# Performance work log

Measured on AMD Instinct MI355X. Metric: run time of the kernel, lower is better.

## Reference

```python
import jax, jax.numpy as jnp
import numpy as np

DECAY = 0.99
EPSILON = 1e-05
CODEBOOK_SIZE = 1024


def setup_inputs() -> dict:
    key = jax.random.key(0)
    k1, k2, k3 = jax.random.split(key, 3)
    B, T, D, K = 8, 4096, 128, CODEBOOK_SIZE
    return {
        "x": jax.random.normal(k1, (B, T, D), dtype=jnp.float32),
        "embed": jax.random.normal(k2, (K, D), dtype=jnp.float32),
        "cluster_size": jnp.ones((K,), dtype=jnp.float32),
        "embed_avg": jax.random.normal(k3, (K, D), dtype=jnp.float32),
    }


def reference(x, embed, cluster_size, embed_avg):
    shape = x.shape
    K, D = embed.shape
    flat = x.reshape(-1, D)  # (N, D)

    dist = 2.0 * (flat @ embed.T) - jnp.sum(flat * flat, axis=1, keepdims=True) \
           - jnp.sum(embed * embed, axis=1)[None, :]  # (N, K)
    embed_ind_flat = jnp.argmax(dist, axis=-1)  # (N,) int
    embed_ind = embed_ind_flat.reshape(shape[:-1])
    quantize = embed[embed_ind]  # dequantize via gather, (B, T, D)

    # training EMA updates (one-hot scatter expressed as segment sums)
    counts = jax.ops.segment_sum(jnp.ones_like(embed_ind_flat, dtype=x.dtype),
                                 embed_ind_flat, num_segments=K)  # == onehot.sum(0)
    embed_sum = jax.ops.segment_sum(flat, embed_ind_flat, num_segments=K)  # == (x.T @ onehot).T

    new_cluster_size = cluster_size * DECAY + (1.0 - DECAY) * counts
    new_embed_avg = embed_avg * DECAY + (1.0 - DECAY) * embed_sum

    total = new_cluster_size.sum()
    smoothed = (new_cluster_size + EPSILON) / (total + K * EPSILON) * total
    new_embed = new_embed_avg / smoothed[:, None]

    return quantize, embed_ind, new_cluster_size, new_embed_avg, new_embed
```

## Files before the change

kernel.cpp:

```cpp
#include <hip/hip_runtime.h>

#define NROWS 32768
#define DDIM  128
#define KCODES 1024
#define DECAY 0.99f
#define OMD   0.01f
#define EPS   1e-5f

typedef __attribute__((ext_vector_type(8))) short short8;
typedef __attribute__((ext_vector_type(4))) float f32x4;

#define WS_COUNTS 0
#define WS_OFFS   1024
#define WS_CURSOR 2048
#define WS_INV    3072
#define WS_EN2H   4096
#define WS_BUCKET 5120

__device__ __forceinline__ unsigned int f2bf(float f) {
  union { float f; unsigned int u; } cv; cv.f = f;
  unsigned int u = cv.u;
  return (u + 0x7fffu + ((u >> 16) & 1u)) >> 16;
}

__device__ __forceinline__ void gload16(const void* g, void* l) {
  __builtin_amdgcn_global_load_lds(
      (const __attribute__((address_space(1))) unsigned int*)g,
      (__attribute__((address_space(3))) unsigned int*)l, 16, 0, 0);
}

__global__ __launch_bounds__(256) void pack_e(const float* __restrict__ embed,
                                              ushort* __restrict__ epack,
                                              float* __restrict__ en2h,
                                              int* __restrict__ cnt0) {
  const int tid = threadIdx.x;
  const int nt = blockIdx.x;
  if (nt == 0) {
    #pragma unroll
    for (int i = 0; i < 4; ++i) cnt0[tid + i * 256] = 0;
  }
  const int m = tid >> 4, s = tid & 15;
  const int kb = s >> 2, q = s & 3;
  const int row = nt * 16 + m;
  const float* ep = embed + (size_t)row * DDIM + kb * 32 + q * 8;
  float4 v0 = *(const float4*)(ep);
  float4 v1 = *(const float4*)(ep + 4);
  float v[8] = {v0.x, v0.y, v0.z, v0.w, v1.x, v1.y, v1.z, v1.w};
  unsigned int h[8], l[8];
  float ss = 0.f;
  #pragma unroll
  for (int j = 0; j < 8; ++j) {
    ss += v[j] * v[j];
    h[j] = f2bf(v[j]);
    float fh = __uint_as_float(h[j] << 16);
    l[j] = f2bf(v[j] - fh);
  }
  uint4 ph, pl;
  ph.x = h[0] | (h[1] << 16); ph.y = h[2] | (h[3] << 16);
  ph.z = h[4] | (h[5] << 16); ph.w = h[6] | (h[7] << 16);
  pl.x = l[0] | (l[1] << 16); pl.y = l[2] | (l[3] << 16);
  pl.z = l[4] | (l[5] << 16); pl.w = l[6] | (l[7] << 16);
  *(uint4*)(epack + (((size_t)nt * 8 + kb) * 64 + q * 16 + m) * 8)     = ph;
  *(uint4*)(epack + (((size_t)nt * 8 + kb + 4) * 64 + q * 16 + m) * 8) = pl;
  ss += __shfl_xor(ss, 1, 64);
  ss += __shfl_xor(ss, 2, 64);
  ss += __shfl_xor(ss, 4, 64);
  ss += __shfl_xor(ss, 8, 64);
  if (s == 0) en2h[row] = 0.5f * ss;
}

__global__ __launch_bounds__(512, 2) void vq_mfma(
    const float* __restrict__ x, const short8* __restrict__ ep8,
    const float* __restrict__ en2h, const float* __restrict__ embed,
    float* __restrict__ out_ind, float* __restrict__ out_q,
    int* __restrict__ cnt_i) {
  __shared__ short8 bfrag[2][512];
  __shared__ float nlds[KCODES];
  __shared__ int scodes[128];
  const int tid = threadIdx.x;
  const int w = tid >> 6, lane = tid & 63;
  const int c = lane & 15, q = lane >> 4;
  const int row0 = blockIdx.x * 128;

  gload16(ep8 + w * 64 + lane, &bfrag[0][w * 64]);
  nlds[tid]       = en2h[tid];
  nlds[tid + 512] = en2h[tid + 512];

  short8 a[8];
  {
    const float* xp = x + (size_t)(row0 + w * 16 + c) * DDIM + q * 8;
    #pragma unroll
    for (int kb = 0; kb < 4; ++kb) {
      float4 v0 = *(const float4*)(xp + kb * 32);
      float4 v1 = *(const float4*)(xp + kb * 32 + 4);
      float v[8] = {v0.x, v0.y, v0.z, v0.w, v1.x, v1.y, v1.z, v1.w};
      short8 hh, ll;
      #pragma unroll
      for (int j = 0; j < 8; ++j) {
        unsigned int hv = f2bf(v[j]);
        hh[j] = (short)hv;
        float fh = __uint_as_float(hv << 16);
        ll[j] = (short)f2bf(v[j] - fh);
      }
      a[kb] = hh;
      a[kb + 4] = ll;
    }
  }

  float bestv[4]; int besti[4];
  #pragma unroll
  for (int i = 0; i < 4; ++i) { bestv[i] = -3.4e38f; besti[i] = 0; }

  asm volatile("s_waitcnt vmcnt(0)" ::: "memory");
  __syncthreads();

  for (int nt = 0; nt < 64; ++nt) {
    const int cur = nt & 1;
    if (nt < 63)
      gload16(ep8 + (size_t)(nt + 1) * 512 + w * 64 + lane,
              &bfrag[cur ^ 1][w * 64]);
    __builtin_amdgcn_sched_barrier(0);

    short8 st[8];
    #pragma unroll
    for (int j = 0; j < 8; ++j) st[j] = bfrag[cur][j * 64 + lane];
    const float nh = nlds[nt * 16 + c];

    f32x4 accA = {-nh, -nh, -nh, -nh};
    f32x4 accB = {0.f, 0.f, 0.f, 0.f};
    f32x4 accC = {0.f, 0.f, 0.f, 0.f};
    __builtin_amdgcn_s_setprio(1);
    #pragma unroll
    for (int kb = 0; kb < 4; ++kb) {
      accA = __builtin_amdgcn_mfma_f32_16x16x32_bf16(a[kb],     st[kb],     accA, 0, 0, 0);
      accB = __builtin_amdgcn_mfma_f32_16x16x32_bf16(a[kb + 4], st[kb],     accB, 0, 0, 0);
      accC = __builtin_amdgcn_mfma_f32_16x16x32_bf16(a[kb],     st[kb + 4], accC, 0, 0, 0);
    }
    __builtin_amdgcn_s_setprio(0);

    const int code = nt * 16 + c;
    #pragma unroll
    for (int r = 0; r < 4; ++r) {
      float s = accA[r] + accB[r] + accC[r];
      if (s > bestv[r]) { bestv[r] = s; besti[r] = code; }
    }

    asm volatile("s_waitcnt vmcnt(0)" ::: "memory");
    __syncthreads();
  }

  #pragma unroll
  for (int off = 1; off < 16; off <<= 1) {
    #pragma unroll
    for (int i = 0; i < 4; ++i) {
      float ov = __shfl_xor(bestv[i], off, 64);
      int   oi = __shfl_xor(besti[i], off, 64);
      if (ov > bestv[i] || (ov == bestv[i] && oi < besti[i])) {
        bestv[i] = ov; besti[i] = oi;
      }
    }
  }
  if (c == 0) {
    #pragma unroll
    for (int r = 0; r < 4; ++r) {
      const int row = w * 16 + q * 4 + r;
      out_ind[row0 + row] = (float)besti[r];
      scodes[row] = besti[r];
      atomicAdd(&cnt_i[besti[r]], 1);
    }
  }
  __syncthreads();
  #pragma unroll
  for (int it = 0; it < 8; ++it) {
    int idx = tid + it * 512;
    int row = idx >> 5, c4 = idx & 31;
    int code = scodes[row];
    *(float4*)(out_q + (size_t)(row0 + row) * DDIM + c4 * 4) =
        *(const float4*)(embed + (size_t)code * DDIM + c4 * 4);
  }
}

__global__ __launch_bounds__(1024) void scan_fin(
    int* offs, const float* __restrict__ cs,
    float* __restrict__ counts_g, int* __restrict__ cursor,
    float* __restrict__ inv, float* __restrict__ out_ncs) {
  __shared__ float wtot[16], ctot[16];
  const int tid = threadIdx.x;
  const int lane = tid & 63, w = tid >> 6;
  const int cnt = offs[tid];
  const float cnum = (float)cnt;
  const float cv = cs[tid];
  float s = cnum;
  #pragma unroll
  for (int off = 1; off < 64; off <<= 1) {
    float v = __shfl_up(s, off, 64);
    if (lane >= off) s += v;
  }
  float r2 = cv;
  #pragma unroll
  for (int off = 32; off > 0; off >>= 1) r2 += __shfl_down(r2, off, 64);
  if (lane == 63) wtot[w] = s;
  if (lane == 0)  ctot[w] = r2;
  __syncthreads();
  if (tid < 16) {
    float v = wtot[tid];
    #pragma unroll
    for (int off = 1; off < 16; off <<= 1) {
      float p = __shfl_up(v, off, 64);
      if (tid >= off) v += p;
    }
    wtot[tid] = v;
    float t2 = ctot[tid];
    #pragma unroll
    for (int off = 8; off > 0; off >>= 1) t2 += __shfl_down(t2, off, 64);
    if (tid == 0) ctot[0] = t2;
  }
  __syncthreads();
  const float prefix = (w > 0) ? wtot[w - 1] : 0.f;
  const int excl = (int)(s + prefix) - cnt;
  offs[tid] = excl;
  cursor[tid] = excl;
  counts_g[tid] = cnum;
  const float ncs = cv * DECAY + OMD * cnum;
  out_ncs[tid] = ncs;
  const float total = ctot[0] * DECAY + OMD * (float)NROWS;
  inv[tid] = (total + (float)KCODES * EPS) / ((ncs + EPS) * total);
}

__global__ void scatter_rows(const float* __restrict__ out_ind,
                             int* __restrict__ cursor, int* __restrict__ bucket) {
  int row = blockIdx.x * 256 + threadIdx.x;
  int code = (int)out_ind[row];
  int pos = atomicAdd(cursor + code, 1);
  bucket[pos] = row;
}

__global__ __launch_bounds__(256) void esum_fin(
    const int* __restrict__ bucket, const int* __restrict__ offs,
    const float* __restrict__ counts, const float* __restrict__ x,
    const float* __restrict__ ea, const float* __restrict__ inv,
    float* __restrict__ out_nea, float* __restrict__ out_ne) {
  __shared__ float4 part[512];
  const int code = blockIdx.x;
  const int t = threadIdx.x;
  const int c8 = t & 15;
  const int h = t >> 4;
  const int start = offs[code];
  const int cnt = (int)counts[code];
  float4 a0 = {0.f, 0.f, 0.f, 0.f}, a1 = {0.f, 0.f, 0.f, 0.f};
  int i = h;
  for (; i + 16 < cnt; i += 32) {
    int rowA = bucket[start + i];
    int rowB = bucket[start + i + 16];
    const float* pa = x + (size_t)rowA * DDIM + c8 * 8;
    const float* pb = x + (size_t)rowB * DDIM + c8 * 8;
    float4 xa0 = *(const float4*)(pa), xa1 = *(const float4*)(pa + 4);
    float4 xb0 = *(const float4*)(pb), xb1 = *(const float4*)(pb + 4);
    a0.x += xa0.x + xb0.x; a0.y += xa0.y + xb0.y; a0.z += xa0.z + xb0.z; a0.w += xa0.w + xb0.w;
    a1.x += xa1.x + xb1.x; a1.y += xa1.y + xb1.y; a1.z += xa1.z + xb1.z; a1.w += xa1.w + xb1.w;
  }
  for (; i < cnt; i += 16) {
    int row = bucket[start + i];
    const float* pa = x + (size_t)row * DDIM + c8 * 8;
    float4 xa0 = *(const float4*)(pa), xa1 = *(const float4*)(pa + 4);
    a0.x += xa0.x; a0.y += xa0.y; a0.z += xa0.z; a0.w += xa0.w;
    a1.x += xa1.x; a1.y += xa1.y; a1.z += xa1.z; a1.w += xa1.w;
  }
  part[h * 32 + c8 * 2]     = a0;
  part[h * 32 + c8 * 2 + 1] = a1;
  __syncthreads();
  if (t < 32) {
    float4 s = part[t];
    #pragma unroll
    for (int hh = 1; hh < 16; ++hh) {
      float4 p = part[hh * 32 + t];
      s.x += p.x; s.y += p.y; s.z += p.z; s.w += p.w;
    }
    float iv = inv[code];
    int base = code * DDIM + t * 4;
    float4 a = *(const float4*)(ea + base);
    float4 nea;
    nea.x = a.x * DECAY + OMD * s.x; nea.y = a.y * DECAY + OMD * s.y;
    nea.z = a.z * DECAY + OMD * s.z; nea.w = a.w * DECAY + OMD * s.w;
    *(float4*)(out_nea + base) = nea;
    float4 ne;
    ne.x = nea.x * iv; ne.y = nea.y * iv; ne.z = nea.z * iv; ne.w = nea.w * iv;
    *(float4*)(out_ne + base) = ne;
  }
}

extern "C" void kernel_launch(void* const* d_in, const int* in_sizes, int n_in,
                              void* d_out, int out_size, void* d_ws, size_t ws_size,
                              hipStream_t stream) {
  const float* x     = (const float*)d_in[0];
  const float* embed = (const float*)d_in[1];
  const float* cs    = (const float*)d_in[2];
  const float* ea    = (const float*)d_in[3];

  float* out     = (float*)d_out;
  float* out_q   = out;
  float* out_ind = out_q + 4194304;
  float* out_ncs = out_ind + 32768;
  float* out_nea = out_ncs + 1024;
  float* out_ne  = out_nea + 131072;

  float* ws     = (float*)d_ws;
  float* counts = ws + WS_COUNTS;
  int*   offs   = (int*)(ws + WS_OFFS);
  int*   cursor = (int*)(ws + WS_CURSOR);
  float* inv    = ws + WS_INV;
  float* en2h   = ws + WS_EN2H;
  int*   bucket = (int*)(ws + WS_BUCKET);

  ushort* epack = (ushort*)out_nea;

  pack_e<<<64, 256, 0, stream>>>(embed, epack, en2h, offs);
  vq_mfma<<<NROWS / 128, 512, 0, stream>>>(x, (const short8*)epack, en2h, embed,
                                           out_ind, out_q, offs);
  scan_fin<<<1, 1024, 0, stream>>>(offs, cs, counts, cursor, inv, out_ncs);
  scatter_rows<<<NROWS / 256, 256, 0, stream>>>(out_ind, cursor, bucket);
  esum_fin<<<KCODES, 256, 0, stream>>>(bucket, offs, counts, x, ea, inv,
                                       out_nea, out_ne);
}
```

Measured before the change: 187.2 us.

## Halve vq block threads, give each wave two row tiles, deepen codebook prefetch

The distance kernel now runs 256 threads per block, and each wave handles 32 rows (two 16-row A tiles). Each B fragment loaded from LDS therefore feeds twice as many MFMAs. The codebook staging buffer grows from double to quad buffering, with a 3-tile-ahead prefetch throttled by vmcnt and raw s_barrier instead of a full wait-plus-syncthreads every tile. The aim is to cut LDS reads and barrier stalls per MFMA, at the cost of more registers per thread and fewer waves per block.

```diff
diff --git a/kernel.cpp b/kernel.cpp
--- a/kernel.cpp
+++ b/kernel.cpp
@@ -69,12 +69,12 @@
   if (s == 0) en2h[row] = 0.5f * ss;
 }
 
-__global__ __launch_bounds__(512, 2) void vq_mfma(
+__global__ __launch_bounds__(256, 2) void vq_mfma(
     const float* __restrict__ x, const short8* __restrict__ ep8,
     const float* __restrict__ en2h, const float* __restrict__ embed,
     float* __restrict__ out_ind, float* __restrict__ out_q,
     int* __restrict__ cnt_i) {
-  __shared__ short8 bfrag[2][512];
+  __shared__ short8 bfrag[4][512];
   __shared__ float nlds[KCODES];
   __shared__ int scodes[128];
   const int tid = threadIdx.x;
@@ -82,13 +82,12 @@
   const int c = lane & 15, q = lane >> 4;
   const int row0 = blockIdx.x * 128;
 
-  gload16(ep8 + w * 64 + lane, &bfrag[0][w * 64]);
-  nlds[tid]       = en2h[tid];
-  nlds[tid + 512] = en2h[tid + 512];
-
-  short8 a[8];
-  {
-    const float* xp = x + (size_t)(row0 + w * 16 + c) * DDIM + q * 8;
+  float4 nv = *(const float4*)(en2h + tid * 4);
+
+  short8 a[2][8];
+  #pragma unroll
+  for (int t = 0; t < 2; ++t) {
+    const float* xp = x + (size_t)(row0 + w * 32 + t * 16 + c) * DDIM + q * 8;
     #pragma unroll
     for (int kb = 0; kb < 4; ++kb) {
       float4 v0 = *(const float4*)(xp + kb * 32);
@@ -102,57 +101,83 @@
         float fh = __uint_as_float(hv << 16);
         ll[j] = (short)f2bf(v[j] - fh);
       }
-      a[kb] = hh;
-      a[kb + 4] = ll;
-    }
-  }
-
-  float bestv[4]; int besti[4];
-  #pragma unroll
-  for (int i = 0; i < 4; ++i) { bestv[i] = -3.4e38f; besti[i] = 0; }
-
-  asm volatile("s_waitcnt vmcnt(0)" ::: "memory");
-  __syncthreads();
-
-  for (int nt = 0; nt < 64; ++nt) {
-    const int cur = nt & 1;
-    if (nt < 63)
-      gload16(ep8 + (size_t)(nt + 1) * 512 + w * 64 + lane,
-              &bfrag[cur ^ 1][w * 64]);
-    __builtin_amdgcn_sched_barrier(0);
-
+      a[t][kb] = hh;
+      a[t][kb + 4] = ll;
+    }
+  }
+  *(float4*)(&nlds[tid * 4]) = nv;
+
+  #pragma unroll
+  for (int p = 0; p < 3; ++p) {
+    gload16(ep8 + (size_t)p * 512 + w * 64 + lane, &bfrag[p][w * 64]);
+    gload16(ep8 + (size_t)p * 512 + 256 + w * 64 + lane, &bfrag[p][256 + w * 64]);
+  }
+  asm volatile("s_waitcnt lgkmcnt(0)" ::: "memory");
+
+  float bestv[8]; int besti[8];
+  #pragma unroll
+  for (int i = 0; i < 8; ++i) { bestv[i] = -3.4e38f; besti[i] = 0; }
+
+  auto tile_compute = [&](int nt) {
+    const int cur = nt & 3;
     short8 st[8];
     #pragma unroll
     for (int j = 0; j < 8; ++j) st[j] = bfrag[cur][j * 64 + lane];
     const float nh = nlds[nt * 16 + c];
-
-    f32x4 accA = {-nh, -nh, -nh, -nh};
-    f32x4 accB = {0.f, 0.f, 0.f, 0.f};
-    f32x4 accC = {0.f, 0.f, 0.f, 0.f};
+    f32x4 accA0 = {-nh, -nh, -nh, -nh};
+    f32x4 accA1 = accA0;
+    f32x4 accB0 = {0.f, 0.f, 0.f, 0.f};
+    f32x4 accB1 = {0.f, 0.f, 0.f, 0.f};
+    f32x4 accC0 = {0.f, 0.f, 0.f, 0.f};
+    f32x4 accC1 = {0.f, 0.f, 0.f, 0.f};
     __builtin_amdgcn_s_setprio(1);
     #pragma unroll
     for (int kb = 0; kb < 4; ++kb) {
-      accA = __builtin_amdgcn_mfma_f32_16x16x32_bf16(a[kb],     st[kb],     accA, 0, 0, 0);
-      accB = __builtin_amdgcn_mfma_f32_16x16x32_bf16(a[kb + 4], st[kb],     accB, 0, 0, 0);
-      accC = __builtin_amdgcn_mfma_f32_16x16x32_bf16(a[kb],     st[kb + 4], accC, 0, 0, 0);
+      accA0 = __builtin_amdgcn_mfma_f32_16x16x32_bf16(a[0][kb],     st[kb],     accA0, 0, 0, 0);
+      accA1 = __builtin_amdgcn_mfma_f32_16x16x32_bf16(a[1][kb],     st[kb],     accA1, 0, 0, 0);
+      accB0 = __builtin_amdgcn_mfma_f32_16x16x32_bf16(a[0][kb + 4], st[kb],     accB0, 0, 0, 0);
+      accB1 = __builtin_amdgcn_mfma_f32_16x16x32_bf16(a[1][kb + 4], st[kb],     accB1, 0, 0, 0);
+      accC0 = __builtin_amdgcn_mfma_f32_16x16x32_bf16(a[0][kb],     st[kb + 4], accC0, 0, 0, 0);
+      accC1 = __builtin_amdgcn_mfma_f32_16x16x32_bf16(a[1][kb],     st[kb + 4], accC1, 0, 0, 0);
     }
     __builtin_amdgcn_s_setprio(0);
-
     const int code = nt * 16 + c;
     #pragma unroll
     for (int r = 0; r < 4; ++r) {
-      float s = accA[r] + accB[r] + accC[r];
-      if (s > bestv[r]) { bestv[r] = s; besti[r] = code; }
-    }
-
-    asm volatile("s_waitcnt vmcnt(0)" ::: "memory");
-    __syncthreads();
-  }
+      float s0 = accA0[r] + accB0[r] + accC0[r];
+      if (s0 > bestv[r])     { bestv[r] = s0;     besti[r] = code; }
+      float s1 = accA1[r] + accB1[r] + accC1[r];
+      if (s1 > bestv[4 + r]) { bestv[4 + r] = s1; besti[4 + r] = code; }
+    }
+  };
+
+  for (int nt = 0; nt < 61; ++nt) {
+    asm volatile("s_waitcnt vmcnt(4)" ::: "memory");
+    __builtin_amdgcn_s_barrier();
+    __builtin_amdgcn_sched_barrier(0);
+    const int bs = (nt + 3) & 3;
+    gload16(ep8 + (size_t)(nt + 3) * 512 + w * 64 + lane, &bfrag[bs][w * 64]);
+    gload16(ep8 + (size_t)(nt + 3) * 512 + 256 + w * 64 + lane, &bfrag[bs][256 + w * 64]);
+    __builtin_amdgcn_sched_barrier(0);
+    tile_compute(nt);
+  }
+  asm volatile("s_waitcnt vmcnt(4)" ::: "memory");
+  __builtin_amdgcn_s_barrier();
+  __builtin_amdgcn_sched_barrier(0);
+  tile_compute(61);
+  asm volatile("s_waitcnt vmcnt(2)" ::: "memory");
+  __builtin_amdgcn_s_barrier();
+  __builtin_amdgcn_sched_barrier(0);
+  tile_compute(62);
+  asm volatile("s_waitcnt vmcnt(0)" ::: "memory");
+  __builtin_amdgcn_s_barrier();
+  __builtin_amdgcn_sched_barrier(0);
+  tile_compute(63);
 
   #pragma unroll
   for (int off = 1; off < 16; off <<= 1) {
     #pragma unroll
-    for (int i = 0; i < 4; ++i) {
+    for (int i = 0; i < 8; ++i) {
       float ov = __shfl_xor(bestv[i], off, 64);
       int   oi = __shfl_xor(besti[i], off, 64);
       if (ov > bestv[i] || (ov == bestv[i] && oi < besti[i])) {
@@ -162,17 +187,20 @@
   }
   if (c == 0) {
     #pragma unroll
-    for (int r = 0; r < 4; ++r) {
-      const int row = w * 16 + q * 4 + r;
-      out_ind[row0 + row] = (float)besti[r];
-      scodes[row] = besti[r];
-      atomicAdd(&cnt_i[besti[r]], 1);
-    }
+    for (int t = 0; t < 2; ++t)
+      #pragma unroll
+      for (int r = 0; r < 4; ++r) {
+        const int row = w * 32 + t * 16 + q * 4 + r;
+        const int bi = besti[t * 4 + r];
+        out_ind[row0 + row] = (float)bi;
+        scodes[row] = bi;
+        atomicAdd(&cnt_i[bi], 1);
+      }
   }
   __syncthreads();
   #pragma unroll
-  for (int it = 0; it < 8; ++it) {
-    int idx = tid + it * 512;
+  for (int it = 0; it < 16; ++it) {
+    int idx = tid + it * 256;
     int row = idx >> 5, c4 = idx & 31;
     int code = scodes[row];
     *(float4*)(out_q + (size_t)(row0 + row) * DDIM + c4 * 4) =
@@ -315,7 +343,7 @@
   ushort* epack = (ushort*)out_nea;
 
   pack_e<<<64, 256, 0, stream>>>(embed, epack, en2h, offs);
-  vq_mfma<<<NROWS / 128, 512, 0, stream>>>(x, (const short8*)epack, en2h, embed,
+  vq_mfma<<<NROWS / 128, 256, 0, stream>>>(x, (const short8*)epack, en2h, embed,
                                            out_ind, out_q, offs);
   scan_fin<<<1, 1024, 0, stream>>>(offs, cs, counts, cursor, inv, out_ncs);
   scatter_rows<<<NROWS / 256, 256, 0, stream>>>(out_ind, cursor, bucket);
```

Result: no change. 190.6 us (+1.8%).

## Split codebook across wave halves with 4-stage prefetch and merge argmax keys

Applied to the files above, without the earlier changes.

The VQ kernel now processes 64 rows per block instead of 128. The two halves of its 8 waves each scan half of the codebook (32 tiles), so twice as many blocks run and each wave does half the serial tile loop. Codebook fragments are prefetched through a 4-deep LDS ring with counted vmcnt waits and raw s_barrier, replacing the double buffer that waited on every load each iteration. The per-half argmax results are merged through packed 64-bit order-preserving keys that keep lowest-index tie-breaking. Launch bounds ask for 4 blocks per CU, which caps registers and raises LDS use per block.

```diff
diff --git a/kernel.cpp b/kernel.cpp
--- a/kernel.cpp
+++ b/kernel.cpp
@@ -69,26 +69,25 @@
   if (s == 0) en2h[row] = 0.5f * ss;
 }
 
-__global__ __launch_bounds__(512, 2) void vq_mfma(
+__global__ __launch_bounds__(512, 4) void vq_mfma(
     const float* __restrict__ x, const short8* __restrict__ ep8,
     const float* __restrict__ en2h, const float* __restrict__ embed,
     float* __restrict__ out_ind, float* __restrict__ out_q,
     int* __restrict__ cnt_i) {
-  __shared__ short8 bfrag[2][512];
+  __shared__ short8 bfrag[2][4][512];
   __shared__ float nlds[KCODES];
-  __shared__ int scodes[128];
+  __shared__ unsigned long long keys[2][64];
+  __shared__ int scodes[64];
   const int tid = threadIdx.x;
   const int w = tid >> 6, lane = tid & 63;
+  const int h = w >> 2, r = w & 3;
   const int c = lane & 15, q = lane >> 4;
-  const int row0 = blockIdx.x * 128;
-
-  gload16(ep8 + w * 64 + lane, &bfrag[0][w * 64]);
-  nlds[tid]       = en2h[tid];
-  nlds[tid + 512] = en2h[tid + 512];
+  const int row0 = blockIdx.x * 64;
+  const int nt0 = h * 32;
 
   short8 a[8];
   {
-    const float* xp = x + (size_t)(row0 + w * 16 + c) * DDIM + q * 8;
+    const float* xp = x + (size_t)(row0 + r * 16 + c) * DDIM + q * 8;
     #pragma unroll
     for (int kb = 0; kb < 4; ++kb) {
       float4 v0 = *(const float4*)(xp + kb * 32);
@@ -106,26 +105,28 @@
       a[kb + 4] = ll;
     }
   }
+  nlds[tid]       = en2h[tid];
+  nlds[tid + 512] = en2h[tid + 512];
+
+  __builtin_amdgcn_sched_barrier(0);
+  #pragma unroll
+  for (int p = 0; p < 3; ++p) {
+    gload16(ep8 + (size_t)(nt0 + p) * 512 + r * 128 + lane,
+            &bfrag[h][p][r * 128]);
+    gload16(ep8 + (size_t)(nt0 + p) * 512 + r * 128 + 64 + lane,
+            &bfrag[h][p][r * 128 + 64]);
+  }
+  asm volatile("s_waitcnt lgkmcnt(0)" ::: "memory");
 
   float bestv[4]; int besti[4];
   #pragma unroll
   for (int i = 0; i < 4; ++i) { bestv[i] = -3.4e38f; besti[i] = 0; }
 
-  asm volatile("s_waitcnt vmcnt(0)" ::: "memory");
-  __syncthreads();
-
-  for (int nt = 0; nt < 64; ++nt) {
-    const int cur = nt & 1;
-    if (nt < 63)
-      gload16(ep8 + (size_t)(nt + 1) * 512 + w * 64 + lane,
-              &bfrag[cur ^ 1][w * 64]);
-    __builtin_amdgcn_sched_barrier(0);
-
+  auto tile_compute = [&](int t) {
     short8 st[8];
     #pragma unroll
-    for (int j = 0; j < 8; ++j) st[j] = bfrag[cur][j * 64 + lane];
-    const float nh = nlds[nt * 16 + c];
-
+    for (int j = 0; j < 8; ++j) st[j] = bfrag[h][t & 3][j * 64 + lane];
+    const float nh = nlds[(nt0 + t) * 16 + c];
     f32x4 accA = {-nh, -nh, -nh, -nh};
     f32x4 accB = {0.f, 0.f, 0.f, 0.f};
     f32x4 accC = {0.f, 0.f, 0.f, 0.f};
@@ -137,17 +138,38 @@
       accC = __builtin_amdgcn_mfma_f32_16x16x32_bf16(a[kb],     st[kb + 4], accC, 0, 0, 0);
     }
     __builtin_amdgcn_s_setprio(0);
-
-    const int code = nt * 16 + c;
-    #pragma unroll
-    for (int r = 0; r < 4; ++r) {
-      float s = accA[r] + accB[r] + accC[r];
-      if (s > bestv[r]) { bestv[r] = s; besti[r] = code; }
-    }
-
-    asm volatile("s_waitcnt vmcnt(0)" ::: "memory");
-    __syncthreads();
-  }
+    const int code = (nt0 + t) * 16 + c;
+    #pragma unroll
+    for (int rr = 0; rr < 4; ++rr) {
+      float s = accA[rr] + accB[rr] + accC[rr];
+      if (s > bestv[rr]) { bestv[rr] = s; besti[rr] = code; }
+    }
+  };
+
+  for (int t = 0; t < 29; ++t) {
+    asm volatile("s_waitcnt vmcnt(4)" ::: "memory");
+    __builtin_amdgcn_s_barrier();
+    __builtin_amdgcn_sched_barrier(0);
+    const int bs = (t + 3) & 3;
+    gload16(ep8 + (size_t)(nt0 + t + 3) * 512 + r * 128 + lane,
+            &bfrag[h][bs][r * 128]);
+    gload16(ep8 + (size_t)(nt0 + t + 3) * 512 + r * 128 + 64 + lane,
+            &bfrag[h][bs][r * 128 + 64]);
+    __builtin_amdgcn_sched_barrier(0);
+    tile_compute(t);
+  }
+  asm volatile("s_waitcnt vmcnt(4)" ::: "memory");
+  __builtin_amdgcn_s_barrier();
+  __builtin_amdgcn_sched_barrier(0);
+  tile_compute(29);
+  asm volatile("s_waitcnt vmcnt(2)" ::: "memory");
+  __builtin_amdgcn_s_barrier();
+  __builtin_amdgcn_sched_barrier(0);
+  tile_compute(30);
+  asm volatile("s_waitcnt vmcnt(0)" ::: "memory");
+  __builtin_amdgcn_s_barrier();
+  __builtin_amdgcn_sched_barrier(0);
+  tile_compute(31);
 
   #pragma unroll
   for (int off = 1; off < 16; off <<= 1) {
@@ -162,16 +184,26 @@
   }
   if (c == 0) {
     #pragma unroll
-    for (int r = 0; r < 4; ++r) {
-      const int row = w * 16 + q * 4 + r;
-      out_ind[row0 + row] = (float)besti[r];
-      scodes[row] = besti[r];
-      atomicAdd(&cnt_i[besti[r]], 1);
-    }
-  }
-  __syncthreads();
-  #pragma unroll
-  for (int it = 0; it < 8; ++it) {
+    for (int rr = 0; rr < 4; ++rr) {
+      unsigned u = __float_as_uint(bestv[rr]);
+      unsigned su = (u & 0x80000000u) ? ~u : (u | 0x80000000u);
+      keys[h][r * 16 + q * 4 + rr] =
+          ((unsigned long long)su << 32) |
+          (unsigned long long)(0xFFFFFFFFu - (unsigned)besti[rr]);
+    }
+  }
+  __syncthreads();
+  if (tid < 64) {
+    unsigned long long k0 = keys[0][tid], k1 = keys[1][tid];
+    unsigned long long k = k0 > k1 ? k0 : k1;
+    int code = (int)(0xFFFFFFFFu - (unsigned)(k & 0xFFFFFFFFull));
+    out_ind[row0 + tid] = (float)code;
+    scodes[tid] = code;
+    atomicAdd(&cnt_i[code], 1);
+  }
+  __syncthreads();
+  #pragma unroll
+  for (int it = 0; it < 4; ++it) {
     int idx = tid + it * 512;
     int row = idx >> 5, c4 = idx & 31;
     int code = scodes[row];
@@ -315,8 +347,8 @@
   ushort* epack = (ushort*)out_nea;
 
   pack_e<<<64, 256, 0, stream>>>(embed, epack, en2h, offs);
-  vq_mfma<<<NROWS / 128, 512, 0, stream>>>(x, (const short8*)epack, en2h, embed,
-                                           out_ind, out_q, offs);
+  vq_mfma<<<NROWS / 64, 512, 0, stream>>>(x, (const short8*)epack, en2h, embed,
+                                          out_ind, out_q, offs);
   scan_fin<<<1, 1024, 0, stream>>>(offs, cs, counts, cursor, inv, out_ncs);
   scatter_rows<<<NROWS / 256, 256, 0, stream>>>(out_ind, cursor, bucket);
   esum_fin<<<KCODES, 256, 0, stream>>>(bucket, offs, counts, x, ea, inv,
```

Result: faster. 168.0 us (-10.2%).

## Load codebook fragments directly into registers with triple-buffered prefetch, drop LDS and barriers

Applied to the files above, without the earlier changes.

The codebook fragments are no longer staged through LDS with global_load_lds and a block barrier on every tile. Each wave now loads its B fragments and norm terms straight from global memory (L2-resident) into registers, using a three-deep software pipeline. Blocks shrink to 256 threads and 64 rows, doubling the grid. This removes 64 per-tile __syncthreads and the LDS traffic, but every wave now fetches the full codebook itself, which raises L2/global load traffic and register pressure.

```diff
diff --git a/kernel.cpp b/kernel.cpp
--- a/kernel.cpp
+++ b/kernel.cpp
@@ -21,12 +21,6 @@
   union { float f; unsigned int u; } cv; cv.f = f;
   unsigned int u = cv.u;
   return (u + 0x7fffu + ((u >> 16) & 1u)) >> 16;
-}
-
-__device__ __forceinline__ void gload16(const void* g, void* l) {
-  __builtin_amdgcn_global_load_lds(
-      (const __attribute__((address_space(1))) unsigned int*)g,
-      (__attribute__((address_space(3))) unsigned int*)l, 16, 0, 0);
 }
 
 __global__ __launch_bounds__(256) void pack_e(const float* __restrict__ embed,
@@ -69,22 +63,16 @@
   if (s == 0) en2h[row] = 0.5f * ss;
 }
 
-__global__ __launch_bounds__(512, 2) void vq_mfma(
+__global__ __launch_bounds__(256, 2) void vq_mfma(
     const float* __restrict__ x, const short8* __restrict__ ep8,
     const float* __restrict__ en2h, const float* __restrict__ embed,
     float* __restrict__ out_ind, float* __restrict__ out_q,
     int* __restrict__ cnt_i) {
-  __shared__ short8 bfrag[2][512];
-  __shared__ float nlds[KCODES];
-  __shared__ int scodes[128];
+  __shared__ int scodes[64];
   const int tid = threadIdx.x;
   const int w = tid >> 6, lane = tid & 63;
   const int c = lane & 15, q = lane >> 4;
-  const int row0 = blockIdx.x * 128;
-
-  gload16(ep8 + w * 64 + lane, &bfrag[0][w * 64]);
-  nlds[tid]       = en2h[tid];
-  nlds[tid + 512] = en2h[tid + 512];
+  const int row0 = blockIdx.x * 64;
 
   short8 a[8];
   {
@@ -111,21 +99,14 @@
   #pragma unroll
   for (int i = 0; i < 4; ++i) { bestv[i] = -3.4e38f; besti[i] = 0; }
 
-  asm volatile("s_waitcnt vmcnt(0)" ::: "memory");
-  __syncthreads();
-
-  for (int nt = 0; nt < 64; ++nt) {
-    const int cur = nt & 1;
-    if (nt < 63)
-      gload16(ep8 + (size_t)(nt + 1) * 512 + w * 64 + lane,
-              &bfrag[cur ^ 1][w * 64]);
-    __builtin_amdgcn_sched_barrier(0);
-
-    short8 st[8];
-    #pragma unroll
-    for (int j = 0; j < 8; ++j) st[j] = bfrag[cur][j * 64 + lane];
-    const float nh = nlds[nt * 16 + c];
-
+  auto stage = [&](short8 (&st)[8], float& nh, int t) {
+    const short8* p = ep8 + (size_t)t * 512 + lane;
+    #pragma unroll
+    for (int j = 0; j < 8; ++j) st[j] = p[j * 64];
+    nh = en2h[t * 16 + c];
+  };
+
+  auto proc = [&](const short8 (&st)[8], float nh, int t) {
     f32x4 accA = {-nh, -nh, -nh, -nh};
     f32x4 accB = {0.f, 0.f, 0.f, 0.f};
     f32x4 accC = {0.f, 0.f, 0.f, 0.f};
@@ -137,17 +118,31 @@
       accC = __builtin_amdgcn_mfma_f32_16x16x32_bf16(a[kb],     st[kb + 4], accC, 0, 0, 0);
     }
     __builtin_amdgcn_s_setprio(0);
-
-    const int code = nt * 16 + c;
+    const int code = t * 16 + c;
     #pragma unroll
     for (int r = 0; r < 4; ++r) {
       float s = accA[r] + accB[r] + accC[r];
       if (s > bestv[r]) { bestv[r] = s; besti[r] = code; }
     }
-
-    asm volatile("s_waitcnt vmcnt(0)" ::: "memory");
-    __syncthreads();
-  }
+  };
+
+  short8 sA[8], sB[8], sC[8];
+  float nhA, nhB, nhC;
+  stage(sA, nhA, 0);
+  stage(sB, nhB, 1);
+
+  for (int t = 0; t < 63; t += 3) {
+    stage(sC, nhC, t + 2);
+    __builtin_amdgcn_sched_barrier(0);
+    proc(sA, nhA, t);
+    stage(sA, nhA, t + 3);
+    __builtin_amdgcn_sched_barrier(0);
+    proc(sB, nhB, t + 1);
+    stage(sB, nhB, (t + 4 > 63) ? 63 : t + 4);
+    __builtin_amdgcn_sched_barrier(0);
+    proc(sC, nhC, t + 2);
+  }
+  proc(sA, nhA, 63);
 
   #pragma unroll
   for (int off = 1; off < 16; off <<= 1) {
@@ -172,7 +167,7 @@
   __syncthreads();
   #pragma unroll
   for (int it = 0; it < 8; ++it) {
-    int idx = tid + it * 512;
+    int idx = tid + it * 256;
     int row = idx >> 5, c4 = idx & 31;
     int code = scodes[row];
     *(float4*)(out_q + (size_t)(row0 + row) * DDIM + c4 * 4) =
@@ -315,8 +310,8 @@
   ushort* epack = (ushort*)out_nea;
 
   pack_e<<<64, 256, 0, stream>>>(embed, epack, en2h, offs);
-  vq_mfma<<<NROWS / 128, 512, 0, stream>>>(x, (const short8*)epack, en2h, embed,
-                                           out_ind, out_q, offs);
+  vq_mfma<<<NROWS / 64, 256, 0, stream>>>(x, (const short8*)epack, en2h, embed,
+                                          out_ind, out_q, offs);
   scan_fin<<<1, 1024, 0, stream>>>(offs, cs, counts, cursor, inv, out_ncs);
   scatter_rows<<<NROWS / 256, 256, 0, stream>>>(out_ind, cursor, bucket);
   esum_fin<<<KCODES, 256, 0, stream>>>(bucket, offs, counts, x, ea, inv,
```

Measured after the change: 167.2 us. -10.7%, faster.
